# Performance work log

Measured on AMD Instinct MI355X. Metric: run time of the kernel, lower is better.

## Reference

```python
import jax, jax.numpy as jnp
import numpy as np
from jax import lax

KS = 3
PAD = 1
N = KS * KS


def setup_inputs() -> dict:
    key = jax.random.key(0)
    k1, k2, k3, k4, k5, k6 = jax.random.split(key, 6)
    b, cin, cout, h, w = 4, 64, 64, 256, 256
    x = jax.random.normal(k1, (b, cin, h, w), jnp.float32)
    # offset-predicting conv: 2*N output channels, 3x3, pad 1
    p_conv_w = 0.1 * jax.random.normal(k2, (2 * N, cin, KS, KS), jnp.float32)
    p_conv_b = jnp.zeros((2 * N,), jnp.float32)
    # main conv applied to the k*k-expanded sampled map (no bias in original)
    conv_w = jax.random.normal(k3, (cout, cin, KS, KS), jnp.float32) / np.sqrt(cin * N)
    bn_gamma = 1.0 + 0.1 * jax.random.normal(k4, (cout,), jnp.float32)
    bn_beta = 0.1 * jax.random.normal(k5, (cout,), jnp.float32)
    return {"x": x, "p_conv_w": p_conv_w, "p_conv_b": p_conv_b,
            "conv_w": conv_w, "bn_gamma": bn_gamma, "bn_beta": bn_beta}


def _deform_conv(x, p_conv_w, p_conv_b, conv_w, bn_gamma, bn_beta):
    b, c, h, w = x.shape
    # offsets: (b, 2N, h, w) -> (b, h, w, 2N)
    offset = lax.conv_general_dilated(x, p_conv_w, (1, 1), ((PAD, PAD), (PAD, PAD)))
    offset = offset + p_conv_b[None, :, None, None]
    offset = jnp.transpose(offset, (0, 2, 3, 1))
    # zero-pad input; sampling coordinates live on the padded grid
    x_pad = jnp.pad(x, ((0, 0), (0, 0), (PAD, PAD), (PAD, PAD)))
    Hp, Wp = h + 2 * PAD, w + 2 * PAD
    # p = p_0 + p_n + offset  (x/y coords each of shape (b,h,w,N))
    r = jnp.arange(-(KS - 1) // 2, KS // 2 + 1, dtype=jnp.float32)  # [-1,0,1]
    pn_x, pn_y = jnp.meshgrid(r, r, indexing="ij")
    pn_x, pn_y = pn_x.reshape(-1), pn_y.reshape(-1)  # (N,)
    p0_x = jnp.arange(1, h + 1, dtype=jnp.float32)[:, None, None]  # (h,1,1)
    p0_y = jnp.arange(1, w + 1, dtype=jnp.float32)[None, :, None]  # (1,w,1)
    p_x = offset[..., :N] + p0_x + pn_x  # (b,h,w,N)
    p_y = offset[..., N:] + p0_y + pn_y
    # integer corner coords (detached / non-differentiable), clamped
    fx = jnp.floor(lax.stop_gradient(p_x))
    fy = jnp.floor(lax.stop_gradient(p_y))
    q_lt_x = jnp.clip(fx, 0, Hp - 1).astype(jnp.int32)
    q_lt_y = jnp.clip(fy, 0, Wp - 1).astype(jnp.int32)
    q_rb_x = jnp.clip(fx + 1, 0, Hp - 1).astype(jnp.int32)
    q_rb_y = jnp.clip(fy + 1, 0, Wp - 1).astype(jnp.int32)
    # clamped continuous coords (gradient flows to offsets)
    px = jnp.clip(p_x, 0, Hp - 1)
    py = jnp.clip(p_y, 0, Wp - 1)
    # bilinear weights
    ltx = q_lt_x.astype(px.dtype); lty = q_lt_y.astype(px.dtype)
    rbx = q_rb_x.astype(px.dtype); rby = q_rb_y.astype(px.dtype)
    g_lt = (1 + (ltx - px)) * (1 + (lty - py))
    g_rb = (1 - (rbx - px)) * (1 - (rby - py))
    g_lb = (1 + (ltx - px)) * (1 - (rby - py))
    g_rt = (1 - (rbx - px)) * (1 + (lty - py))
    x_flat = x_pad.reshape(b, c, Hp * Wp)

    def gather(qx, qy):
        idx = (qx * Wp + qy).reshape(b, 1, -1)  # (b,1,h*w*N)
        out = jnp.take_along_axis(x_flat, idx, axis=2)
        return out.reshape(b, c, h, w, N)

    x_off = (g_lt[:, None] * gather(q_lt_x, q_lt_y)
             + g_rb[:, None] * gather(q_rb_x, q_rb_y)
             + g_lb[:, None] * gather(q_lt_x, q_rb_y)
             + g_rt[:, None] * gather(q_rb_x, q_lt_y))  # (b,c,h,w,N)
    # conv (kernel=KS, stride=KS on k*k-expanded map) == contraction over (c,N)
    out = jnp.einsum("bchwn,ocn->bohw", x_off, conv_w.reshape(conv_w.shape[0], c, N))
    # BatchNorm2d (training-mode batch statistics) + LeakyReLU(0.1)
    mean = out.mean(axis=(0, 2, 3), keepdims=True)
    var = out.var(axis=(0, 2, 3), keepdims=True)
    y = (out - mean) * lax.rsqrt(var + 1e-5)
    y = y * bn_gamma[None, :, None, None] + bn_beta[None, :, None, None]
    return jnp.where(y > 0, y, 0.1 * y)


def reference(x, p_conv_w, p_conv_b, conv_w, bn_gamma, bn_beta):
    return _deform_conv(x, p_conv_w, p_conv_b, conv_w, bn_gamma, bn_beta)
```

## Files before the change

kernel.cpp:

```cpp
#include <hip/hip_runtime.h>
#include <math.h>

#define BB 4
#define CC 64
#define OCC 64
#define HH 256
#define WW 256
#define HP 258
#define WP 258
#define NPIX (BB * HH * WW)
#define CNT_F 262144.0f

typedef __attribute__((ext_vector_type(8))) __bf16 bf16x8;
typedef __attribute__((ext_vector_type(4))) float f32x4;

__device__ __forceinline__ float blo(unsigned u) {
    return __builtin_bit_cast(float, u << 16);
}
__device__ __forceinline__ float bhi(unsigned u) {
    return __builtin_bit_cast(float, u & 0xffff0000u);
}

__global__ __launch_bounds__(256) void prep(const float* __restrict__ x,
                                            __bf16* __restrict__ xt,
                                            const float* __restrict__ cw,
                                            const float* __restrict__ pw,
                                            __bf16* __restrict__ wtb,
                                            __bf16* __restrict__ pwb,
                                            float* __restrict__ stats) {
    int blk = blockIdx.x;
    int tid = threadIdx.x;
    if (blk < 4096) {
        int xchunk = blk & 3;
        int y = (blk >> 2) & 255;
        int b = blk >> 10;
        __shared__ float tile[64][65];
        int x0 = xchunk * 64;
        int col = tid & 63;
        int crow = tid >> 6;
        const float* xp = x + ((size_t)b * CC) * HH * WW + (size_t)y * WW + x0;
#pragma unroll
        for (int i = 0; i < 16; ++i) {
            int c = crow + i * 4;
            tile[c][col] = xp[(size_t)c * HH * WW + col];
        }
        __syncthreads();
        __bf16* op = xt + (((size_t)b * HP + (y + 1)) * WP + (x0 + 1)) * CC;
#pragma unroll
        for (int i = 0; i < 16; ++i) {
            int xl = crow + i * 4;
            op[(size_t)xl * CC + col] = (__bf16)tile[col][xl];
        }
    } else if (blk < 5124) {
        int i = (blk - 4096) * 256 + tid;
        const int total = BB * 1028 * CC;
        if (i >= total) return;
        int c = i & 63;
        int p = (i >> 6) % 1028;
        int b = (i >> 6) / 1028;
        int yp, xp;
        if (p < 258)      { yp = 0;           xp = p; }
        else if (p < 516) { yp = 257;         xp = p - 258; }
        else if (p < 772) { yp = p - 516 + 1; xp = 0; }
        else              { yp = p - 772 + 1; xp = 257; }
        xt[(((size_t)b * HP + yp) * WP + xp) * CC + c] = (__bf16)0.0f;
    } else if (blk < 5340) {
        int i = (blk - 5124) * 256 + tid;
        if (i < 36864) {
            int c = i & 63;
            int n = (i >> 6) % 9;
            int oc = i / 576;
            wtb[i] = (__bf16)cw[((size_t)oc * CC + c) * 9 + n];
        } else {
            int j = i - 36864;
            if (j >= 18432) return;
            int c = j & 63;
            int n = (j >> 6) % 9;
            int oc = j / 576;
            pwb[j] = (__bf16)(oc < 18 ? pw[((size_t)oc * CC + c) * 9 + n] : 0.0f);
        }
    } else {
        if (tid < 128) stats[tid] = 0.0f;
    }
}

__global__ __launch_bounds__(256, 7) void deform_fused(const __bf16* __restrict__ xt,
                                                       const __bf16* __restrict__ pwb,
                                                       const float* __restrict__ pb,
                                                       const __bf16* __restrict__ wtb,
                                                       float* __restrict__ out,
                                                       float* __restrict__ partials) {
    int phys = blockIdx.x;
    int blk = (phys & 7) * 2048 + (phys >> 3);
    int xh = blk & 15;
    int y  = (blk >> 4) & 255;
    int b  = blk >> 12;
    int x0 = xh * 16;
    int tid = threadIdx.x;
    int wave = tid >> 6, lane = tid & 63;
    int chp = lane & 31, half = lane >> 5;

    __shared__ __attribute__((aligned(16))) char smem[20736];
    __bf16 (*sS)[18][72] = (__bf16 (*)[18][72])smem;
    char* sAb = smem;
    float* offp = (float*)(smem + 18432);

    {
        const char* base = (const char*)xt + (size_t)b * HP * WP * CC * 2;
        for (int t = tid; t < 432; t += 256) {
            int pos = t >> 3, c8 = t & 7;
            int r = pos / 18, j = pos - r * 18;
            uint4 d = *(const uint4*)(base
                + (size_t)((y + r) * WP + (x0 + j)) * (CC * 2) + c8 * 16);
            *(uint4*)&sS[r][j][c8 * 8] = d;
        }
    }
    __syncthreads();

    {
        int nh = wave & 1;
        int kh = wave >> 1;
        int m = lane & 15, q = lane >> 4;
        f32x4 acc = {0.0f, 0.0f, 0.0f, 0.0f};
        const __bf16* bp = pwb + (size_t)(nh * 16 + m) * 576 + q * 8;
        if (kh == 0) {
#pragma unroll
            for (int n = 0; n < 5; ++n) {
                int dy = n / 3, dx = n - dy * 3;
                const __bf16* abase = &sS[dy][m + dx][q * 8];
#pragma unroll
                for (int h = 0; h < 2; ++h) {
                    bf16x8 a  = *(const bf16x8*)(abase + h * 32);
                    bf16x8 bv = *(const bf16x8*)(bp + n * 64 + h * 32);
                    acc = __builtin_amdgcn_mfma_f32_16x16x32_bf16(a, bv, acc, 0, 0, 0);
                }
            }
        } else {
#pragma unroll
            for (int n = 5; n < 9; ++n) {
                int dy = n / 3, dx = n - dy * 3;
                const __bf16* abase = &sS[dy][m + dx][q * 8];
#pragma unroll
                for (int h = 0; h < 2; ++h) {
                    bf16x8 a  = *(const bf16x8*)(abase + h * 32);
                    bf16x8 bv = *(const bf16x8*)(bp + n * 64 + h * 32);
                    acc = __builtin_amdgcn_mfma_f32_16x16x32_bf16(a, bv, acc, 0, 0, 0);
                }
            }
        }
        int oc = nh * 16 + m;
        if (oc < 18) {
            float bias = (kh == 0) ? pb[oc] : 0.0f;
            float* obf = offp + kh * 288;
#pragma unroll
            for (int r = 0; r < 4; ++r)
                obf[(q * 4 + r) * 18 + oc] = acc[r] + bias;
        }
    }
    __syncthreads();

    float g0 = 0.0f, g1 = 0.0f, g2 = 0.0f, g3 = 0.0f;
    int c0 = 0, c1 = 0, c2 = 0, c3 = 0;
    if (lane < 36) {
        int t = wave * 36 + lane;
        int n = t >> 4, p = t & 15;
        float offx = offp[p * 18 + n]     + offp[288 + p * 18 + n];
        float offy = offp[p * 18 + n + 9] + offp[288 + p * 18 + n + 9];
        float px = offx + (float)(y + 1) + (float)(n / 3 - 1);
        float py = offy + (float)(x0 + p + 1) + (float)(n % 3 - 1);
        float fx = floorf(px), fy = floorf(py);
        float pxc = fminf(fmaxf(px, 0.0f), 257.0f);
        float pyc = fminf(fmaxf(py, 0.0f), 257.0f);
        int ltx = (int)fminf(fmaxf(fx, 0.0f), 257.0f);
        int lty = (int)fminf(fmaxf(fy, 0.0f), 257.0f);
        int rbx = (int)fminf(fmaxf(fx + 1.0f, 0.0f), 257.0f);
        int rby = (int)fminf(fmaxf(fy + 1.0f, 0.0f), 257.0f);
        float dxl = 1.0f + ((float)ltx - pxc);
        float dxr = 1.0f - ((float)rbx - pxc);
        float dyl = 1.0f + ((float)lty - pyc);
        float dyr = 1.0f - ((float)rby - pyc);
        g0 = dxl * dyl;
        g1 = dxr * dyr;
        g2 = dxl * dyr;
        g3 = dxr * dyl;
        c0 = ((ltx * WP + lty) * CC) * 2;
        c1 = ((rbx * WP + rby) * CC) * 2;
        c2 = ((ltx * WP + rby) * CC) * 2;
        c3 = ((rbx * WP + lty) * CC) * 2;
    }

    {
        const char* xbl = (const char*)xt + (size_t)b * HP * WP * CC * 2 + (size_t)chp * 4;
#pragma unroll 3
        for (int r = 0; r < 18; ++r) {
            int src = r * 2 + half;
            float gx = __shfl(g0, src, 64);
            float gy = __shfl(g1, src, 64);
            float gz = __shfl(g2, src, 64);
            float gw = __shfl(g3, src, 64);
            int vx = __shfl(c0, src, 64);
            int vy = __shfl(c1, src, 64);
            int vz = __shfl(c2, src, 64);
            int vw = __shfl(c3, src, 64);
            unsigned d0 = *(const unsigned*)(xbl + vx);
            unsigned d1 = *(const unsigned*)(xbl + vy);
            unsigned d2 = *(const unsigned*)(xbl + vz);
            unsigned d3 = *(const unsigned*)(xbl + vw);
            float lo = gx * blo(d0) + gy * blo(d1) + gz * blo(d2) + gw * blo(d3);
            float hi = gx * bhi(d0) + gy * bhi(d1) + gz * bhi(d2) + gw * bhi(d3);
            __bf16 rlo = (__bf16)lo, rhi = (__bf16)hi;
            ushort2 rv;
            rv.x = __builtin_bit_cast(unsigned short, rlo);
            rv.y = __builtin_bit_cast(unsigned short, rhi);
            int t = wave * 36 + src;
            int n = t >> 4, p = t & 15;
            unsigned bo = (unsigned)p * 1152u + (unsigned)n * 128u + (unsigned)chp * 4u;
            bo ^= (unsigned)((p & 7) << 4);
            *(ushort2*)(sAb + bo) = rv;
        }
    }
    __syncthreads();

    int m = lane & 15, q = lane >> 4;
    f32x4 acc = {0.0f, 0.0f, 0.0f, 0.0f};
    {
        unsigned rowb = (unsigned)m * 1152u;
        unsigned key = (unsigned)((m & 7) << 4);
        const __bf16* bp = wtb + (size_t)(wave * 16 + m) * 576 + q * 8;
        __builtin_amdgcn_s_setprio(1);
#pragma unroll
        for (int k0 = 0; k0 < 576; k0 += 32) {
            unsigned bo = rowb + (((unsigned)(k0 * 2 + q * 16)) ^ key);
            bf16x8 a  = *(const bf16x8*)(sAb + bo);
            bf16x8 bv = *(const bf16x8*)(bp + k0);
            acc = __builtin_amdgcn_mfma_f32_16x16x32_bf16(a, bv, acc, 0, 0, 0);
        }
        __builtin_amdgcn_s_setprio(0);
    }

    int oc = wave * 16 + m;
    float* ob = out + (((size_t)b * OCC + oc) * HH + y) * WW + x0 + q * 4;
    float4 v;
    v.x = acc[0]; v.y = acc[1]; v.z = acc[2]; v.w = acc[3];
    *(float4*)ob = v;

    {
        float s  = acc[0] + acc[1] + acc[2] + acc[3];
        float sq = acc[0] * acc[0] + acc[1] * acc[1]
                 + acc[2] * acc[2] + acc[3] * acc[3];
        s  += __shfl_xor(s, 16, 64);
        sq += __shfl_xor(sq, 16, 64);
        s  += __shfl_xor(s, 32, 64);
        sq += __shfl_xor(sq, 32, 64);
        if (q == 0) {
            float* pp = partials + (size_t)phys * 128;
            pp[oc] = s;
            pp[64 + oc] = sq;
        }
    }
}

__global__ __launch_bounds__(256) void stats_reduce(const float* __restrict__ partials,
                                                    float* __restrict__ stats) {
    __shared__ float sacc[8][128];
    int tid = threadIdx.x;
    int cg = tid & 31;
    int rg = tid >> 5;
    float a0 = 0.0f, a1 = 0.0f, a2 = 0.0f, a3 = 0.0f;
    const float* base = partials + ((size_t)blockIdx.x * 256 + rg) * 128 + cg * 4;
#pragma unroll 4
    for (int r = 0; r < 32; ++r) {
        float4 v = *(const float4*)(base + (size_t)r * 8 * 128);
        a0 += v.x; a1 += v.y; a2 += v.z; a3 += v.w;
    }
    sacc[rg][cg * 4 + 0] = a0;
    sacc[rg][cg * 4 + 1] = a1;
    sacc[rg][cg * 4 + 2] = a2;
    sacc[rg][cg * 4 + 3] = a3;
    __syncthreads();
    if (tid < 128) {
        float s = 0.0f;
#pragma unroll
        for (int g = 0; g < 8; ++g) s += sacc[g][tid];
        atomicAdd(&stats[tid], s);
    }
}

__global__ __launch_bounds__(256) void bn_leaky(float* __restrict__ out,
                                                const float* __restrict__ stats,
                                                const float* __restrict__ gamma,
                                                const float* __restrict__ beta) {
    int i = blockIdx.x * 256 + threadIdx.x;
    int oc = (i >> 14) & 63;
    float mean = stats[oc] * (1.0f / CNT_F);
    float var = stats[64 + oc] * (1.0f / CNT_F) - mean * mean;
    float scale = gamma[oc] * rsqrtf(var + 1e-5f);
    float shift = beta[oc] - mean * scale;
    float4* o4 = (float4*)out;
    float4 v = o4[i];
    v.x = v.x * scale + shift; v.x = v.x > 0.0f ? v.x : 0.1f * v.x;
    v.y = v.y * scale + shift; v.y = v.y > 0.0f ? v.y : 0.1f * v.y;
    v.z = v.z * scale + shift; v.z = v.z > 0.0f ? v.z : 0.1f * v.z;
    v.w = v.w * scale + shift; v.w = v.w > 0.0f ? v.w : 0.1f * v.w;
    o4[i] = v;
}

extern "C" void kernel_launch(void* const* d_in, const int* in_sizes, int n_in,
                              void* d_out, int out_size, void* d_ws, size_t ws_size,
                              hipStream_t stream) {
    (void)in_sizes; (void)n_in; (void)out_size; (void)ws_size;
    const float* x     = (const float*)d_in[0];
    const float* pw    = (const float*)d_in[1];
    const float* pb    = (const float*)d_in[2];
    const float* cw    = (const float*)d_in[3];
    const float* gamma = (const float*)d_in[4];
    const float* beta  = (const float*)d_in[5];
    float* out = (float*)d_out;
    char* ws = (char*)d_ws;

    __bf16* xtb  = (__bf16*)ws;
    float* partials = (float*)(ws + 34080768);
    __bf16* wtb  = (__bf16*)(ws + 34080768 + 18874368);
    __bf16* pwb  = (__bf16*)(ws + 34080768 + 18874368 + 73728);
    float*  stats = (float*)(ws + 34080768 + 18874368 + 73728 + 36864);

    prep<<<5341, 256, 0, stream>>>(x, xtb, cw, pw, wtb, pwb, stats);
    deform_fused<<<16384, 256, 0, stream>>>(xtb, pwb, pb, wtb, out, partials);
    stats_reduce<<<64, 256, 0, stream>>>(partials, stats);
    bn_leaky<<<NPIX * OCC / 4 / 256, 256, 0, stream>>>(out, stats, gamma, beta);
}
```

Before: 371.5 us.

## Widen deform tile to 32 pixels with 512-thread blocks; vectorize bf16 transpose stores

```diff
diff --git a/kernel.cpp b/kernel.cpp
--- a/kernel.cpp
+++ b/kernel.cpp
@@ -46,10 +46,21 @@
         }
         __syncthreads();
         __bf16* op = xt + (((size_t)b * HP + (y + 1)) * WP + (x0 + 1)) * CC;
-#pragma unroll
-        for (int i = 0; i < 16; ++i) {
-            int xl = crow + i * 4;
-            op[(size_t)xl * CC + col] = (__bf16)tile[col][xl];
+        int c0 = (tid & 15) * 4;
+        int xg = tid >> 4;
+#pragma unroll
+        for (int i = 0; i < 4; ++i) {
+            int xl = xg + i * 16;
+            __bf16 v0 = (__bf16)tile[c0 + 0][xl];
+            __bf16 v1 = (__bf16)tile[c0 + 1][xl];
+            __bf16 v2 = (__bf16)tile[c0 + 2][xl];
+            __bf16 v3 = (__bf16)tile[c0 + 3][xl];
+            ushort4 rv;
+            rv.x = __builtin_bit_cast(unsigned short, v0);
+            rv.y = __builtin_bit_cast(unsigned short, v1);
+            rv.z = __builtin_bit_cast(unsigned short, v2);
+            rv.w = __builtin_bit_cast(unsigned short, v3);
+            *(ushort4*)&op[(size_t)xl * CC + c0] = rv;
         }
     } else if (blk < 5124) {
         int i = (blk - 4096) * 256 + tid;
@@ -84,32 +95,32 @@
     }
 }
 
-__global__ __launch_bounds__(256, 7) void deform_fused(const __bf16* __restrict__ xt,
+__global__ __launch_bounds__(512, 6) void deform_fused(const __bf16* __restrict__ xt,
                                                        const __bf16* __restrict__ pwb,
                                                        const float* __restrict__ pb,
                                                        const __bf16* __restrict__ wtb,
                                                        float* __restrict__ out,
                                                        float* __restrict__ partials) {
     int phys = blockIdx.x;
-    int blk = (phys & 7) * 2048 + (phys >> 3);
-    int xh = blk & 15;
-    int y  = (blk >> 4) & 255;
-    int b  = blk >> 12;
-    int x0 = xh * 16;
+    int blk = (phys & 7) * 1024 + (phys >> 3);
+    int xq = blk & 7;
+    int y  = (blk >> 3) & 255;
+    int b  = blk >> 11;
+    int x0 = xq * 32;
     int tid = threadIdx.x;
     int wave = tid >> 6, lane = tid & 63;
     int chp = lane & 31, half = lane >> 5;
 
-    __shared__ __attribute__((aligned(16))) char smem[20736];
-    __bf16 (*sS)[18][72] = (__bf16 (*)[18][72])smem;
+    __shared__ __attribute__((aligned(16))) char smem[41472];
+    __bf16 (*sS)[34][72] = (__bf16 (*)[34][72])smem;
     char* sAb = smem;
-    float* offp = (float*)(smem + 18432);
+    float* offp = (float*)(smem + 36864);
 
     {
         const char* base = (const char*)xt + (size_t)b * HP * WP * CC * 2;
-        for (int t = tid; t < 432; t += 256) {
+        for (int t = tid; t < 816; t += 512) {
             int pos = t >> 3, c8 = t & 7;
-            int r = pos / 18, j = pos - r * 18;
+            int r = pos / 34, j = pos - r * 34;
             uint4 d = *(const uint4*)(base
                 + (size_t)((y + r) * WP + (x0 + j)) * (CC * 2) + c8 * 16);
             *(uint4*)&sS[r][j][c8 * 8] = d;
@@ -118,16 +129,18 @@
     __syncthreads();
 
     {
-        int nh = wave & 1;
-        int kh = wave >> 1;
+        int mh = wave & 1;
+        int nh = (wave >> 1) & 1;
+        int kh = wave >> 2;
         int m = lane & 15, q = lane >> 4;
+        int p_a = mh * 16 + m;
         f32x4 acc = {0.0f, 0.0f, 0.0f, 0.0f};
         const __bf16* bp = pwb + (size_t)(nh * 16 + m) * 576 + q * 8;
         if (kh == 0) {
 #pragma unroll
             for (int n = 0; n < 5; ++n) {
                 int dy = n / 3, dx = n - dy * 3;
-                const __bf16* abase = &sS[dy][m + dx][q * 8];
+                const __bf16* abase = &sS[dy][p_a + dx][q * 8];
 #pragma unroll
                 for (int h = 0; h < 2; ++h) {
                     bf16x8 a  = *(const bf16x8*)(abase + h * 32);
@@ -139,7 +152,7 @@
 #pragma unroll
             for (int n = 5; n < 9; ++n) {
                 int dy = n / 3, dx = n - dy * 3;
-                const __bf16* abase = &sS[dy][m + dx][q * 8];
+                const __bf16* abase = &sS[dy][p_a + dx][q * 8];
 #pragma unroll
                 for (int h = 0; h < 2; ++h) {
                     bf16x8 a  = *(const bf16x8*)(abase + h * 32);
@@ -151,10 +164,10 @@
         int oc = nh * 16 + m;
         if (oc < 18) {
             float bias = (kh == 0) ? pb[oc] : 0.0f;
-            float* obf = offp + kh * 288;
+            float* obf = offp + kh * 576;
 #pragma unroll
             for (int r = 0; r < 4; ++r)
-                obf[(q * 4 + r) * 18 + oc] = acc[r] + bias;
+                obf[(mh * 16 + q * 4 + r) * 18 + oc] = acc[r] + bias;
         }
     }
     __syncthreads();
@@ -163,9 +176,9 @@
     int c0 = 0, c1 = 0, c2 = 0, c3 = 0;
     if (lane < 36) {
         int t = wave * 36 + lane;
-        int n = t >> 4, p = t & 15;
-        float offx = offp[p * 18 + n]     + offp[288 + p * 18 + n];
-        float offy = offp[p * 18 + n + 9] + offp[288 + p * 18 + n + 9];
+        int n = t >> 5, p = t & 31;
+        float offx = offp[p * 18 + n]     + offp[576 + p * 18 + n];
+        float offy = offp[p * 18 + n + 9] + offp[576 + p * 18 + n + 9];
         float px = offx + (float)(y + 1) + (float)(n / 3 - 1);
         float py = offy + (float)(x0 + p + 1) + (float)(n % 3 - 1);
         float fx = floorf(px), fy = floorf(py);
@@ -213,7 +226,7 @@
             rv.x = __builtin_bit_cast(unsigned short, rlo);
             rv.y = __builtin_bit_cast(unsigned short, rhi);
             int t = wave * 36 + src;
-            int n = t >> 4, p = t & 15;
+            int n = t >> 5, p = t & 31;
             unsigned bo = (unsigned)p * 1152u + (unsigned)n * 128u + (unsigned)chp * 4u;
             bo ^= (unsigned)((p & 7) << 4);
             *(ushort2*)(sAb + bo) = rv;
@@ -222,11 +235,14 @@
     __syncthreads();
 
     int m = lane & 15, q = lane >> 4;
+    int ph = wave >> 2;
+    int oc = (wave & 3) * 16 + m;
     f32x4 acc = {0.0f, 0.0f, 0.0f, 0.0f};
     {
-        unsigned rowb = (unsigned)m * 1152u;
-        unsigned key = (unsigned)((m & 7) << 4);
-        const __bf16* bp = wtb + (size_t)(wave * 16 + m) * 576 + q * 8;
+        int prow = ph * 16 + m;
+        unsigned rowb = (unsigned)prow * 1152u;
+        unsigned key = (unsigned)((prow & 7) << 4);
+        const __bf16* bp = wtb + (size_t)oc * 576 + q * 8;
         __builtin_amdgcn_s_setprio(1);
 #pragma unroll
         for (int k0 = 0; k0 < 576; k0 += 32) {
@@ -238,8 +254,7 @@
         __builtin_amdgcn_s_setprio(0);
     }
 
-    int oc = wave * 16 + m;
-    float* ob = out + (((size_t)b * OCC + oc) * HH + y) * WW + x0 + q * 4;
+    float* ob = out + (((size_t)b * OCC + oc) * HH + y) * WW + x0 + ph * 16 + q * 4;
     float4 v;
     v.x = acc[0]; v.y = acc[1]; v.z = acc[2]; v.w = acc[3];
     *(float4*)ob = v;
@@ -253,7 +268,7 @@
         s  += __shfl_xor(s, 32, 64);
         sq += __shfl_xor(sq, 32, 64);
         if (q == 0) {
-            float* pp = partials + (size_t)phys * 128;
+            float* pp = partials + ((size_t)phys * 2 + ph) * 128;
             pp[oc] = s;
             pp[64 + oc] = sq;
         }
@@ -325,7 +340,7 @@
     float*  stats = (float*)(ws + 34080768 + 18874368 + 73728 + 36864);
 
     prep<<<5341, 256, 0, stream>>>(x, xtb, cw, pw, wtb, pwb, stats);
-    deform_fused<<<16384, 256, 0, stream>>>(xtb, pwb, pb, wtb, out, partials);
+    deform_fused<<<8192, 512, 0, stream>>>(xtb, pwb, pb, wtb, out, partials);
     stats_reduce<<<64, 256, 0, stream>>>(partials, stats);
     bn_leaky<<<NPIX * OCC / 4 / 256, 256, 0, stream>>>(out, stats, gamma, beta);
 }
```

Measured after the change: 374.4 us (median of 2 runs). No clear change (+0.8%).
